# Kernel tuning notes

Measured on AMD Instinct MI355X. Metric: run time of the kernel, lower is better.

## Reference

```python
import jax, jax.numpy as jnp
import numpy as np

D_IN = 1024
D_OUT = 1024
NUM_HEADS = 16
HEAD_DIM = D_OUT // NUM_HEADS


def setup_inputs() -> dict:
    key = jax.random.key(0)
    k_x, k_q, k_k, k_v, k_o, k_ob = jax.random.split(key, 6)
    s_in = 1.0 / np.sqrt(D_IN)
    s_out = 1.0 / np.sqrt(D_OUT)
    return {
        "x": jax.random.normal(k_x, (4, 2048, D_IN), dtype=jnp.float32),
        "W_Q": jax.random.uniform(k_q, (D_IN, D_OUT), jnp.float32, -s_in, s_in),
        "W_K": jax.random.uniform(k_k, (D_IN, D_OUT), jnp.float32, -s_in, s_in),
        "W_V": jax.random.uniform(k_v, (D_IN, D_OUT), jnp.float32, -s_in, s_in),
        "W_O": jax.random.uniform(k_o, (D_OUT, D_OUT), jnp.float32, -s_out, s_out),
        "b_O": jax.random.uniform(k_ob, (D_OUT,), jnp.float32, -s_out, s_out),
    }


def reference(x, W_Q, W_K, W_V, W_O, b_O):
    B, T, _ = x.shape
    # projections -> [B, H, T, Dh]
    Q = (x @ W_Q).reshape(B, T, NUM_HEADS, HEAD_DIM).transpose(0, 2, 1, 3)
    K = (x @ W_K).reshape(B, T, NUM_HEADS, HEAD_DIM).transpose(0, 2, 1, 3)
    V = (x @ W_V).reshape(B, T, NUM_HEADS, HEAD_DIM).transpose(0, 2, 1, 3)
    scores = jnp.einsum("bhqd,bhkd->bhqk", Q, K) / np.sqrt(HEAD_DIM).astype(np.float32)
    causal = jnp.tril(jnp.ones((T, T), dtype=bool))  # True = keep
    scores = jnp.where(causal, scores, -jnp.inf)
    weights = jax.nn.softmax(scores, axis=-1)
    ctx = jnp.einsum("bhqk,bhkd->bhqd", weights, V)
    ctx = ctx.transpose(0, 2, 1, 3).reshape(B, T, D_OUT)
    return ctx @ W_O + b_O
```

## Files before the change

kernel.cpp:

```cpp
#include <hip/hip_runtime.h>

typedef unsigned short ushort_t;
typedef __attribute__((ext_vector_type(8))) __bf16 bf16x8;
typedef __attribute__((ext_vector_type(4))) float f32x4;
typedef __attribute__((ext_vector_type(16))) float f32x16;
typedef __attribute__((ext_vector_type(4))) unsigned short us4;
typedef __attribute__((ext_vector_type(8))) unsigned short us8;
typedef __attribute__((ext_vector_type(4))) unsigned int u32x4;

#define AS1 __attribute__((address_space(1)))
#define AS3 __attribute__((address_space(3)))

__device__ __forceinline__ unsigned short f2bf(float f) {
    unsigned u = __float_as_uint(f);
    u += 0x7fff + ((u >> 16) & 1);
    return (unsigned short)(u >> 16);
}

__device__ __forceinline__ unsigned cvtpk_bf16(float lo, float hi) {
    unsigned r;
    asm("v_cvt_pk_bf16_f32 %0, %1, %2" : "=v"(r) : "v"(lo), "v"(hi));
    return r;
}

__device__ __forceinline__ float fast_exp2(float x) {
    float r;
    asm("v_exp_f32 %0, %1" : "=v"(r) : "v"(x));
    return r;
}

__global__ void k_convert_x(const float* __restrict__ x, ushort_t* __restrict__ xb, int n4) {
    int i = blockIdx.x * blockDim.x + threadIdx.x;
    int stride = gridDim.x * blockDim.x;
    for (; i < n4; i += stride) {
        float4 f = reinterpret_cast<const float4*>(x)[i];
        us4 o = { f2bf(f.x), f2bf(f.y), f2bf(f.z), f2bf(f.w) };
        reinterpret_cast<us4*>(xb)[i] = o;
    }
}

__global__ void k_transpose_w(const float* __restrict__ wq, const float* __restrict__ wk,
                              const float* __restrict__ wv, const float* __restrict__ wo,
                              ushort_t* __restrict__ wqkvt, ushort_t* __restrict__ wot) {
    __shared__ float t[64][65];
    int bx = blockIdx.x;
    int w = bx >> 8;
    int ti = bx & 255;
    int k0 = (ti >> 4) * 64, n0 = (ti & 15) * 64;
    const float* src = (w == 0) ? wq : (w == 1) ? wk : (w == 2) ? wv : wo;
    ushort_t* dst = (w < 3) ? (wqkvt + (size_t)w * 1048576) : wot;
    for (int i = threadIdx.x; i < 4096; i += 256) {
        int r = i >> 6, c = i & 63;
        t[c][r] = src[(size_t)(k0 + r) * 1024 + n0 + c];
    }
    __syncthreads();
    for (int i = threadIdx.x; i < 4096; i += 256) {
        int r = i >> 6, c = i & 63;
        dst[(size_t)(n0 + r) * 1024 + k0 + c] = f2bf(t[r][c]);
    }
}

__global__ __launch_bounds__(256) void k_gemm_qkv(
    const ushort_t* __restrict__ xb, const ushort_t* __restrict__ wt,
    ushort_t* __restrict__ qd, ushort_t* __restrict__ kd, ushort_t* __restrict__ vd) {
    __shared__ ushort_t lA[128 * 32];
    __shared__ ushort_t lB[128 * 32];
    const int tid = threadIdx.x, wid = tid >> 6, lane = tid & 63;
    const int lr = lane & 15, lg = lane >> 4;
    const int wm = wid >> 1, wn = wid & 1;
    const int bx = blockIdx.x;
    const int by = blockIdx.y;
    const int row0 = by * 128, col0 = bx * 128;
    const int crow = lane >> 2;
    const int coff = (lane & 3) * 8;

    f32x4 acc[4][4] = {};

    for (int k0 = 0; k0 < 1024; k0 += 32) {
        for (int c = wid; c < 8; c += 4) {
            const ushort_t* ga = xb + (size_t)(row0 + c * 16 + crow) * 1024 + k0 + coff;
            __builtin_amdgcn_global_load_lds((const AS1 void*)ga, (AS3 void*)(lA + c * 512), 16, 0, 0);
            const ushort_t* gb = wt + (size_t)(col0 + c * 16 + crow) * 1024 + k0 + coff;
            __builtin_amdgcn_global_load_lds((const AS1 void*)gb, (AS3 void*)(lB + c * 512), 16, 0, 0);
        }
        __syncthreads();
        bf16x8 af[4], bfr[4];
#pragma unroll
        for (int i = 0; i < 4; ++i) {
            af[i]  = *reinterpret_cast<const bf16x8*>(lA + (wm * 64 + i * 16 + lr) * 32 + lg * 8);
            bfr[i] = *reinterpret_cast<const bf16x8*>(lB + (wn * 64 + i * 16 + lr) * 32 + lg * 8);
        }
#pragma unroll
        for (int mi = 0; mi < 4; ++mi)
#pragma unroll
            for (int ni = 0; ni < 4; ++ni)
                acc[mi][ni] = __builtin_amdgcn_mfma_f32_16x16x32_bf16(af[mi], bfr[ni], acc[mi][ni], 0, 0, 0);
        __syncthreads();
    }

    const int w = bx >> 3;
    ushort_t* dst = (w == 0) ? qd : (w == 1) ? kd : vd;
    const float osc = (w == 0) ? 0.18033688f : 1.0f;
#pragma unroll
    for (int mi = 0; mi < 4; ++mi) {
#pragma unroll
        for (int ni = 0; ni < 4; ++ni) {
            int col = col0 + wn * 64 + ni * 16 + lr;
            int c1 = col & 1023;
            int h = c1 >> 6, dh = c1 & 63;
#pragma unroll
            for (int e = 0; e < 4; ++e) {
                int row = row0 + wm * 64 + mi * 16 + lg * 4 + e;
                int b = row >> 11, t = row & 2047;
                dst[(((size_t)(b * 16 + h)) * 2048 + t) * 64 + dh] = f2bf(acc[mi][ni][e] * osc);
            }
        }
    }
}

__global__ __launch_bounds__(256) void k_transpose_v(const ushort_t* __restrict__ vd,
                                                     ushort_t* __restrict__ vt) {
    __shared__ __attribute__((aligned(16))) ushort_t tile[64 * 72];
    int bid = blockIdx.x;
    int bh = bid >> 5, tt = bid & 31;
    const ushort_t* src = vd + ((size_t)bh * 2048 + tt * 64) * 64;
    ushort_t* dst = vt + (size_t)bh * 2048 * 64 + tt * 64;
#pragma unroll
    for (int r = 0; r < 2; ++r) {
        int i = r * 256 + threadIdx.x;
        int t = i >> 3, c8 = (i & 7) * 8;
        us8 v = *reinterpret_cast<const us8*>(src + (size_t)t * 64 + c8);
        *reinterpret_cast<us8*>(&tile[t * 72 + (c8 ^ ((t >> 3) << 3))]) = v;
    }
    __syncthreads();
#pragma unroll
    for (int r = 0; r < 2; ++r) {
        int i = r * 256 + threadIdx.x;
        int dh = i >> 3, t8 = (i & 7) * 8;
        us8 o;
#pragma unroll
        for (int e = 0; e < 8; ++e)
            o[e] = tile[(t8 + e) * 72 + (dh ^ ((t8 >> 3) << 3))];
        *reinterpret_cast<us8*>(dst + (size_t)dh * 2048 + t8) = o;
    }
}

__global__ __launch_bounds__(256) void k_attn(
    const ushort_t* __restrict__ q, const ushort_t* __restrict__ k,
    const ushort_t* __restrict__ v, ushort_t* __restrict__ ctx) {
    __shared__ __attribute__((aligned(16))) ushort_t lsK[2 * 8192];
    __shared__ __attribute__((aligned(16))) ushort_t lsV[2 * 8192];

    const int tid = threadIdx.x, wid = tid >> 6, lane = tid & 63;
    const int l31 = lane & 31, hi = lane >> 5;
    const int bid = blockIdx.x;
    const int bh = bid >> 3, pi = bid & 7;
    const size_t base = (size_t)bh * 2048 * 64;
    const ushort_t* qg = q + base;
    const ushort_t* kg = k + base;
    const ushort_t* vtg = v + base;
    const int b = bh >> 4, h = bh & 15;

    const int skey = wid * 8 + (lane >> 3);
    const int scb0 = ((lane & 7) * 16) ^ ((skey & 7) << 4);
    const int kx = (l31 & 7) << 4;
    int koffA[4];
#pragma unroll
    for (int s = 0; s < 4; ++s)
        koffA[s] = l31 * 128 + ((s * 32 + hi * 16) ^ kx);

    us8 ow;
#pragma unroll
    for (int e = 0; e < 8; ++e) ow[e] = 0x3F80;
    const bf16x8 onef = __builtin_bit_cast(bf16x8, ow);

#pragma unroll 1
    for (int pass = 0; pass < 2; ++pass) {
        const int qt = pass ? pi : (15 - pi);
        const int q0 = qt * 128;
        const int q0w = q0 + wid * 32;
        const int qrow = q0w + l31;
        const int njt = qt + 1;

        bf16x8 qf[4];
#pragma unroll
        for (int s = 0; s < 4; ++s)
            qf[s] = *reinterpret_cast<const bf16x8*>(qg + (size_t)qrow * 64 + s * 16 + hi * 8);

        const ushort_t* kpr[4];
        const ushort_t* vpr[4];
#pragma unroll
        for (int r = 0; r < 4; ++r) {
            kpr[r] = kg + (size_t)(r * 32 + skey) * 64 + (scb0 >> 1);
            vpr[r] = vtg + (size_t)((r & 1) * 32 + skey) * 2048 + (r >> 1) * 64 + (scb0 >> 1);
        }

        f32x16 acc0 = {}, acc1 = {}, lacc = {};

        __syncthreads();
#pragma unroll
        for (int r = 0; r < 4; ++r) {
            __builtin_amdgcn_global_load_lds((const AS1 void*)kpr[r],
                (AS3 void*)((AS3 char*)lsK + r * 4096 + wid * 1024), 16, 0, 0);
            __builtin_amdgcn_global_load_lds((const AS1 void*)vpr[r],
                (AS3 void*)((AS3 char*)lsV + r * 4096 + wid * 1024), 16, 0, 0);
        }

        unsigned bo = 0;
        for (int jt = 0; jt < njt; ++jt) {
            __syncthreads();
            const int j0 = jt << 7;
            if (jt + 1 < njt) {
                const unsigned nb = bo ^ 16384;
#pragma unroll
                for (int r = 0; r < 4; ++r) {
                    kpr[r] += 8192;
                    vpr[r] += 128;
                    __builtin_amdgcn_global_load_lds((const AS1 void*)kpr[r],
                        (AS3 void*)((AS3 char*)lsK + nb + r * 4096 + wid * 1024), 16, 0, 0);
                    __builtin_amdgcn_global_load_lds((const AS1 void*)vpr[r],
                        (AS3 void*)((AS3 char*)lsV + nb + r * 4096 + wid * 1024), 16, 0, 0);
                }
            }

#pragma unroll
            for (int hh = 0; hh < 2; ++hh) {
                const int j0h = j0 + hh * 64;
                if (j0h < q0w + 32) {
                    const char* bK = reinterpret_cast<const char*>(lsK) + bo + hh * 8192;
                    const char* bV = reinterpret_cast<const char*>(lsV) + bo + hh * 8192;

                    f32x16 s0 = {}, s1 = {};
#pragma unroll
                    for (int s = 0; s < 4; ++s) {
                        bf16x8 ka = *reinterpret_cast<const bf16x8*>(bK + koffA[s]);
                        s0 = __builtin_amdgcn_mfma_f32_32x32x16_bf16(ka, qf[s], s0, 0, 0, 0);
                    }
#pragma unroll
                    for (int s = 0; s < 4; ++s) {
                        bf16x8 ka = *reinterpret_cast<const bf16x8*>(bK + 4096 + koffA[s]);
                        s1 = __builtin_amdgcn_mfma_f32_32x32x16_bf16(ka, qf[s], s1, 0, 0, 0);
                    }

                    float p0[16], p1[16];
                    if (j0h + 63 > q0w) {
                        const int jh = j0h + 4 * hi;
#pragma unroll
                        for (int r = 0; r < 16; ++r) {
                            const int kl = jh + (r & 3) + 8 * (r >> 2);
                            float e0 = fast_exp2(s0[r]);
                            float e1 = fast_exp2(s1[r]);
                            p0[r] = (kl > qrow) ? 0.f : e0;
                            p1[r] = (kl + 32 > qrow) ? 0.f : e1;
                        }
                    } else {
#pragma unroll
                        for (int r = 0; r < 16; ++r) {
                            p0[r] = fast_exp2(s0[r]);
                            p1[r] = fast_exp2(s1[r]);
                        }
                    }

#pragma unroll
                    for (int kb = 0; kb < 2; ++kb) {
                        const float* pp = kb ? p1 : p0;
                        unsigned pw[8];
#pragma unroll
                        for (int g = 0; g < 4; ++g) {
                            pw[2 * g]     = cvtpk_bf16(pp[4 * g],     pp[4 * g + 1]);
                            pw[2 * g + 1] = cvtpk_bf16(pp[4 * g + 2], pp[4 * g + 3]);
                        }
#pragma unroll
                        for (int j = 0; j < 2; ++j) {
                            asm("v_permlane32_swap_b32 %0, %1" : "+v"(pw[4 * j]),     "+v"(pw[4 * j + 2]));
                            asm("v_permlane32_swap_b32 %0, %1" : "+v"(pw[4 * j + 1]), "+v"(pw[4 * j + 3]));
                            u32x4 fw = { pw[4 * j], pw[4 * j + 1], pw[4 * j + 2], pw[4 * j + 3] };
                            bf16x8 pf = __builtin_bit_cast(bf16x8, fw);
                            const int jj = kb * 2 + j;
                            {
                                bf16x8 vf = *reinterpret_cast<const bf16x8*>(bV + koffA[jj]);
                                acc0 = __builtin_amdgcn_mfma_f32_32x32x16_bf16(vf, pf, acc0, 0, 0, 0);
                            }
                            {
                                bf16x8 vf = *reinterpret_cast<const bf16x8*>(bV + 4096 + koffA[jj]);
                                acc1 = __builtin_amdgcn_mfma_f32_32x32x16_bf16(vf, pf, acc1, 0, 0, 0);
                            }
                            lacc = __builtin_amdgcn_mfma_f32_32x32x16_bf16(onef, pf, lacc, 0, 0, 0);
                        }
                    }
                }
            }
            bo ^= 16384;
        }

        float inv = 1.0f / lacc[0];
        size_t orow = ((size_t)(b * 2048 + qrow)) * 1024 + h * 64;
#pragma unroll
        for (int g = 0; g < 4; ++g) {
            us4 o0 = { f2bf(acc0[4 * g] * inv),     f2bf(acc0[4 * g + 1] * inv),
                       f2bf(acc0[4 * g + 2] * inv), f2bf(acc0[4 * g + 3] * inv) };
            *reinterpret_cast<us4*>(&ctx[orow + 8 * g + 4 * hi]) = o0;
            us4 o1 = { f2bf(acc1[4 * g] * inv),     f2bf(acc1[4 * g + 1] * inv),
                       f2bf(acc1[4 * g + 2] * inv), f2bf(acc1[4 * g + 3] * inv) };
            *reinterpret_cast<us4*>(&ctx[orow + 32 + 8 * g + 4 * hi]) = o1;
        }
    }
}

__global__ __launch_bounds__(256) void k_gemm_out(
    const ushort_t* __restrict__ cb, const ushort_t* __restrict__ wot,
    const float* __restrict__ bO, float* __restrict__ out) {
    __shared__ ushort_t lA[128 * 32];
    __shared__ ushort_t lB[128 * 32];
    const int tid = threadIdx.x, wid = tid >> 6, lane = tid & 63;
    const int lr = lane & 15, lg = lane >> 4;
    const int wm = wid >> 1, wn = wid & 1;
    const int bx = blockIdx.x;
    const int by = blockIdx.y;
    const int row0 = by * 128, col0 = bx * 128;
    const int crow = lane >> 2;
    const int coff = (lane & 3) * 8;

    f32x4 acc[4][4] = {};

    for (int k0 = 0; k0 < 1024; k0 += 32) {
        for (int c = wid; c < 8; c += 4) {
            const ushort_t* ga = cb + (size_t)(row0 + c * 16 + crow) * 1024 + k0 + coff;
            __builtin_amdgcn_global_load_lds((const AS1 void*)ga, (AS3 void*)(lA + c * 512), 16, 0, 0);
            const ushort_t* gb = wot + (size_t)(col0 + c * 16 + crow) * 1024 + k0 + coff;
            __builtin_amdgcn_global_load_lds((const AS1 void*)gb, (AS3 void*)(lB + c * 512), 16, 0, 0);
        }
        __syncthreads();
        bf16x8 af[4], bfr[4];
#pragma unroll
        for (int i = 0; i < 4; ++i) {
            af[i]  = *reinterpret_cast<const bf16x8*>(lA + (wm * 64 + i * 16 + lr) * 32 + lg * 8);
            bfr[i] = *reinterpret_cast<const bf16x8*>(lB + (wn * 64 + i * 16 + lr) * 32 + lg * 8);
        }
#pragma unroll
        for (int mi = 0; mi < 4; ++mi)
#pragma unroll
            for (int ni = 0; ni < 4; ++ni)
                acc[mi][ni] = __builtin_amdgcn_mfma_f32_16x16x32_bf16(af[mi], bfr[ni], acc[mi][ni], 0, 0, 0);
        __syncthreads();
    }

#pragma unroll
    for (int mi = 0; mi < 4; ++mi) {
#pragma unroll
        for (int ni = 0; ni < 4; ++ni) {
            int col = col0 + wn * 64 + ni * 16 + lr;
            float bias = bO[col];
#pragma unroll
            for (int e = 0; e < 4; ++e) {
                int row = row0 + wm * 64 + mi * 16 + lg * 4 + e;
                out[(size_t)row * 1024 + col] = acc[mi][ni][e] + bias;
            }
        }
    }
}

extern "C" void kernel_launch(void* const* d_in, const int* in_sizes, int n_in,
                              void* d_out, int out_size, void* d_ws, size_t ws_size,
                              hipStream_t stream) {
    const float* x  = (const float*)d_in[0];
    const float* wq = (const float*)d_in[1];
    const float* wk = (const float*)d_in[2];
    const float* wv = (const float*)d_in[3];
    const float* wo = (const float*)d_in[4];
    const float* bo = (const float*)d_in[5];
    float* out = (float*)d_out;

    char* ws = (char*)d_ws;
    ushort_t* xb    = (ushort_t*)(ws);
    ushort_t* wqkvt = (ushort_t*)(ws + 16777216);
    ushort_t* wot   = (ushort_t*)(ws + 23068672);
    ushort_t* qd    = (ushort_t*)(ws + 25165824);
    ushort_t* kd    = (ushort_t*)(ws + 41943040);
    ushort_t* vd    = (ushort_t*)(ws + 58720256);
    ushort_t* cd    = (ushort_t*)(ws + 75497472);
    ushort_t* vt    = xb;

    k_convert_x<<<2048, 256, 0, stream>>>(x, xb, 8192 * 1024 / 4);
    k_transpose_w<<<1024, 256, 0, stream>>>(wq, wk, wv, wo, wqkvt, wot);
    k_gemm_qkv<<<dim3(24, 64), 256, 0, stream>>>(xb, wqkvt, qd, kd, vd);
    k_transpose_v<<<2048, 256, 0, stream>>>(vd, vt);
    k_attn<<<512, 256, 0, stream>>>(qd, kd, vt, cd);
    k_gemm_out<<<dim3(8, 64), 256, 0, stream>>>(cd, wot, bo, out);
}
```

Measured before the change: 176.9 us.

## Rewrite QKV GEMM with 256x256 tiles, double-buffered LDS pipeline and XOR swizzle

Replaces the 128x128, single-buffered QKV projection GEMM with a 256x256-tile, 512-thread kernel. Operand tiles for K step kt+1 and kt+2 are issued in phases and overlap with MFMA work on the current buffer, using explicit vmcnt waits and raw barriers. The kernel also XOR-swizzles the LDS layout to cut bank conflicts, remaps block IDs so neighbouring blocks share operand tiles in cache, and raises MFMA priority with setprio. This targets the synchronous load-compute stalls and low data reuse of the old kernel. In exchange it uses 128 KB of LDS and more accumulator registers, which limits occupancy, and the hand-scheduled wait counts are fragile.

After: 175.1 us. About the same (-1.0%).

```diff
diff --git a/kernel.cpp b/kernel.cpp
--- a/kernel.cpp
+++ b/kernel.cpp
@@ -60,59 +60,140 @@
     }
 }
 
-__global__ __launch_bounds__(256) void k_gemm_qkv(
-    const ushort_t* __restrict__ xb, const ushort_t* __restrict__ wt,
+__global__ __launch_bounds__(512, 2) void k_gemm_qkv256(
+    const ushort_t* __restrict__ A, const ushort_t* __restrict__ Bm,
     ushort_t* __restrict__ qd, ushort_t* __restrict__ kd, ushort_t* __restrict__ vd) {
-    __shared__ ushort_t lA[128 * 32];
-    __shared__ ushort_t lB[128 * 32];
+    __shared__ __attribute__((aligned(16))) ushort_t lds[2 * 32768];
+
     const int tid = threadIdx.x, wid = tid >> 6, lane = tid & 63;
     const int lr = lane & 15, lg = lane >> 4;
-    const int wm = wid >> 1, wn = wid & 1;
-    const int bx = blockIdx.x;
-    const int by = blockIdx.y;
-    const int row0 = by * 128, col0 = bx * 128;
-    const int crow = lane >> 2;
-    const int coff = (lane & 3) * 8;
-
-    f32x4 acc[4][4] = {};
-
-    for (int k0 = 0; k0 < 1024; k0 += 32) {
-        for (int c = wid; c < 8; c += 4) {
-            const ushort_t* ga = xb + (size_t)(row0 + c * 16 + crow) * 1024 + k0 + coff;
-            __builtin_amdgcn_global_load_lds((const AS1 void*)ga, (AS3 void*)(lA + c * 512), 16, 0, 0);
-            const ushort_t* gb = wt + (size_t)(col0 + c * 16 + crow) * 1024 + k0 + coff;
-            __builtin_amdgcn_global_load_lds((const AS1 void*)gb, (AS3 void*)(lB + c * 512), 16, 0, 0);
-        }
-        __syncthreads();
-        bf16x8 af[4], bfr[4];
-#pragma unroll
-        for (int i = 0; i < 4; ++i) {
-            af[i]  = *reinterpret_cast<const bf16x8*>(lA + (wm * 64 + i * 16 + lr) * 32 + lg * 8);
-            bfr[i] = *reinterpret_cast<const bf16x8*>(lB + (wn * 64 + i * 16 + lr) * 32 + lg * 8);
-        }
-#pragma unroll
-        for (int mi = 0; mi < 4; ++mi)
-#pragma unroll
-            for (int ni = 0; ni < 4; ++ni)
-                acc[mi][ni] = __builtin_amdgcn_mfma_f32_16x16x32_bf16(af[mi], bfr[ni], acc[mi][ni], 0, 0, 0);
-        __syncthreads();
-    }
-
-    const int w = bx >> 3;
+    const int wm = wid >> 2, wn = wid & 3;
+
+    int bid = blockIdx.x;
+    int wg = (bid & 7) * 48 + (bid >> 3);
+    const int by = wg / 12, bx = wg % 12;
+    const int row0 = by * 256, col0 = bx * 256;
+
+    const int srcrow = lane >> 2;
+    const int srccol = (((lane & 3) * 16) ^ ((lane >> 5) << 5)) >> 1;
+    const ushort_t* aS = A  + (size_t)(row0 + srcrow) * 1024 + srccol;
+    const ushort_t* bS = Bm + (size_t)(col0 + srcrow) * 1024 + srccol;
+    const int rdoff = (lr * 64 + lg * 16) ^ ((lr >> 3) << 5);
+
+    const int s0 = (wid & 3) + ((wid >> 2) << 3);
+    const int s1 = s0 + 4;
+
+#define STG_A(kt, sr, sc) \
+    __builtin_amdgcn_global_load_lds((const AS1 void*)(aS + (size_t)(sr) * 16384 + (kt) * 64 + (sc) * 32), \
+        (AS3 void*)((AS3 char*)lds + (((kt) & 1) << 16) + (sr) * 2048 + (sc) * 1024), 16, 0, 0)
+#define STG_B(kt, sr, sc) \
+    __builtin_amdgcn_global_load_lds((const AS1 void*)(bS + (size_t)(sr) * 16384 + (kt) * 64 + (sc) * 32), \
+        (AS3 void*)((AS3 char*)lds + (((kt) & 1) << 16) + 32768 + (sr) * 2048 + (sc) * 1024), 16, 0, 0)
+#define ISSUE_P1(kt)  { STG_A(kt, s0, 0); }
+#define ISSUE_P2(kt)  { STG_A(kt, s1, 0); STG_B(kt, 2 * wid, 0); STG_B(kt, 2 * wid + 1, 0); }
+#define ISSUE_P3(kt)  { STG_A(kt, s0, 1); }
+#define ISSUE_TOP(kt) { STG_A(kt, s1, 1); STG_B(kt, 2 * wid, 1); STG_B(kt, 2 * wid + 1, 1); }
+
+    f32x4 acc[8][4] = {};
+
+    ISSUE_P1(0); ISSUE_P2(0); ISSUE_P3(0); ISSUE_TOP(0);
+    ISSUE_P1(1); ISSUE_P2(1); ISSUE_P3(1);
+
+#pragma unroll 1
+    for (int kt = 0; kt < 16; ++kt) {
+        if (kt < 15) {
+            ISSUE_TOP(kt + 1);
+            asm volatile("s_waitcnt vmcnt(8)" ::: "memory");
+        } else {
+            asm volatile("s_waitcnt vmcnt(0)" ::: "memory");
+        }
+        __builtin_amdgcn_s_barrier();
+
+        const char* bufA = (const char*)lds + ((kt & 1) << 16);
+        const char* bufB = bufA + 32768;
+        bf16x8 av[4], bv[4];
+
+#pragma unroll
+        for (int x = 0; x < 4; ++x) {
+            av[x] = *reinterpret_cast<const bf16x8*>(bufA + (wm * 8 + x) * 2048 + rdoff);
+            bv[x] = *reinterpret_cast<const bf16x8*>(bufB + (wn * 4 + x) * 2048 + rdoff);
+        }
+        __builtin_amdgcn_s_setprio(1);
+#pragma unroll
+        for (int mf = 0; mf < 4; ++mf)
+#pragma unroll
+            for (int nf = 0; nf < 4; ++nf)
+                acc[mf][nf] = __builtin_amdgcn_mfma_f32_16x16x32_bf16(av[mf], bv[nf], acc[mf][nf], 0, 0, 0);
+        __builtin_amdgcn_s_setprio(0);
+        asm volatile("s_waitcnt lgkmcnt(0)" ::: "memory");
+        __builtin_amdgcn_s_barrier();
+
+        if (kt < 14) ISSUE_P1(kt + 2);
+#pragma unroll
+        for (int x = 0; x < 4; ++x)
+            av[x] = *reinterpret_cast<const bf16x8*>(bufA + (wm * 8 + 4 + x) * 2048 + rdoff);
+        __builtin_amdgcn_s_setprio(1);
+#pragma unroll
+        for (int mf = 0; mf < 4; ++mf)
+#pragma unroll
+            for (int nf = 0; nf < 4; ++nf)
+                acc[4 + mf][nf] = __builtin_amdgcn_mfma_f32_16x16x32_bf16(av[mf], bv[nf], acc[4 + mf][nf], 0, 0, 0);
+        __builtin_amdgcn_s_setprio(0);
+        asm volatile("s_waitcnt lgkmcnt(0)" ::: "memory");
+        __builtin_amdgcn_s_barrier();
+
+        if (kt < 14) ISSUE_P2(kt + 2);
+#pragma unroll
+        for (int x = 0; x < 4; ++x) {
+            av[x] = *reinterpret_cast<const bf16x8*>(bufA + (wm * 8 + x) * 2048 + 1024 + rdoff);
+            bv[x] = *reinterpret_cast<const bf16x8*>(bufB + (wn * 4 + x) * 2048 + 1024 + rdoff);
+        }
+        __builtin_amdgcn_s_setprio(1);
+#pragma unroll
+        for (int mf = 0; mf < 4; ++mf)
+#pragma unroll
+            for (int nf = 0; nf < 4; ++nf)
+                acc[mf][nf] = __builtin_amdgcn_mfma_f32_16x16x32_bf16(av[mf], bv[nf], acc[mf][nf], 0, 0, 0);
+        __builtin_amdgcn_s_setprio(0);
+        asm volatile("s_waitcnt lgkmcnt(0)" ::: "memory");
+        __builtin_amdgcn_s_barrier();
+
+        if (kt < 14) ISSUE_P3(kt + 2);
+#pragma unroll
+        for (int x = 0; x < 4; ++x)
+            av[x] = *reinterpret_cast<const bf16x8*>(bufA + (wm * 8 + 4 + x) * 2048 + 1024 + rdoff);
+        __builtin_amdgcn_s_setprio(1);
+#pragma unroll
+        for (int mf = 0; mf < 4; ++mf)
+#pragma unroll
+            for (int nf = 0; nf < 4; ++nf)
+                acc[4 + mf][nf] = __builtin_amdgcn_mfma_f32_16x16x32_bf16(av[mf], bv[nf], acc[4 + mf][nf], 0, 0, 0);
+        __builtin_amdgcn_s_setprio(0);
+        asm volatile("s_waitcnt lgkmcnt(0)" ::: "memory");
+        __builtin_amdgcn_s_barrier();
+    }
+#undef STG_A
+#undef STG_B
+#undef ISSUE_P1
+#undef ISSUE_P2
+#undef ISSUE_P3
+#undef ISSUE_TOP
+
+    const int w = bx >> 2;
     ushort_t* dst = (w == 0) ? qd : (w == 1) ? kd : vd;
     const float osc = (w == 0) ? 0.18033688f : 1.0f;
 #pragma unroll
-    for (int mi = 0; mi < 4; ++mi) {
-#pragma unroll
-        for (int ni = 0; ni < 4; ++ni) {
-            int col = col0 + wn * 64 + ni * 16 + lr;
+    for (int mi = 0; mi < 8; ++mi) {
+#pragma unroll
+        for (int nf = 0; nf < 4; ++nf) {
+            int col = col0 + wn * 64 + nf * 16 + lr;
             int c1 = col & 1023;
             int h = c1 >> 6, dh = c1 & 63;
 #pragma unroll
             for (int e = 0; e < 4; ++e) {
-                int row = row0 + wm * 64 + mi * 16 + lg * 4 + e;
+                int row = row0 + wm * 128 + mi * 16 + lg * 4 + e;
                 int b = row >> 11, t = row & 2047;
-                dst[(((size_t)(b * 16 + h)) * 2048 + t) * 64 + dh] = f2bf(acc[mi][ni][e] * osc);
+                dst[(((size_t)(b * 16 + h)) * 2048 + t) * 64 + dh] = f2bf(acc[mi][nf][e] * osc);
             }
         }
     }
@@ -383,7 +464,7 @@
 
     k_convert_x<<<2048, 256, 0, stream>>>(x, xb, 8192 * 1024 / 4);
     k_transpose_w<<<1024, 256, 0, stream>>>(wq, wk, wv, wo, wqkvt, wot);
-    k_gemm_qkv<<<dim3(24, 64), 256, 0, stream>>>(xb, wqkvt, qd, kd, vd);
+    k_gemm_qkv256<<<384, 512, 0, stream>>>(xb, wqkvt, qd, kd, vd);
     k_transpose_v<<<2048, 256, 0, stream>>>(vd, vt);
     k_attn<<<512, 256, 0, stream>>>(qd, kd, vt, cd);
     k_gemm_out<<<dim3(8, 64), 256, 0, stream>>>(cd, wot, bo, out);
```
